# Kernel optimization log

Measured on AMD Instinct MI355X. Metric: run time of the kernel, lower is better.

Reference implementation:

```python
import jax, jax.numpy as jnp
import numpy as np

N_NODES = 50000
N_EDGES = 800000
D_IN = 256
D_OUT = 96


def setup_inputs() -> dict:
    key = jax.random.key(0)
    k1, k2, k3 = jax.random.split(key, 3)
    x = jax.random.normal(k1, (N_NODES, D_IN), dtype=jnp.float32)
    edge_index = jax.random.randint(k2, (2, N_EDGES), 0, N_NODES, dtype=jnp.int64)
    # Glorot-like init for the GCN weight, zeros bias (bias_init=zeros_)
    W = jax.random.normal(k3, (D_IN, D_OUT), dtype=jnp.float32) * (1.0 / np.sqrt(D_IN))
    b = jnp.zeros((D_OUT,), dtype=jnp.float32)
    return {"x": x, "edge_index": edge_index, "W": W, "b": b}


def reference(x, edge_index, W, b):
    # GCNConv with normalize=False, add_self_loops=False:
    #   h = x @ W                      [N, D_OUT]
    #   out[dst] = sum over edges of h[src]
    #   out += bias (added after aggregation)
    src, dst = edge_index[0], edge_index[1]
    h = x @ W                                  # dense projection [N, D_OUT]
    msgs = h[src]                              # gather [E, D_OUT]
    out = jax.ops.segment_sum(msgs, dst, num_segments=x.shape[0])  # scatter-add
    return out + b
```

## Files before the change

### kernel.cpp

```cpp
#include <hip/hip_runtime.h>
#include <hip/hip_bf16.h>

#define N_NODES 50000
#define N_EDGES 800000
#define D_IN 256
#define D_OUT 96

#define NBLK 391
#define NTHR 512
#define CAP  2560
#define EPB  ((N_EDGES + NBLK - 1) / NBLK)
#define EPT  ((EPB + NTHR - 1) / NTHR)
#define WLDS_K 264

typedef short bf16x8 __attribute__((ext_vector_type(8)));
typedef float f32x4 __attribute__((ext_vector_type(4)));

static __device__ inline ushort f2bf(float f) {
    union { __hip_bfloat16 h; ushort s; } u;
    u.h = __float2bfloat16(f);
    return u.s;
}
static __device__ inline float bfhi2f(unsigned int hibits) {
    union { unsigned int u; float f; } v; v.u = hibits; return v.f;
}

__global__ __launch_bounds__(256) void gcn_wt_kernel(
    const float* __restrict__ W, ushort* __restrict__ wT,
    int* __restrict__ bucket_cursor) {
    int c = blockIdx.x;
    int k = threadIdx.x;
    wT[c * D_IN + k] = f2bf(W[k * D_OUT + c]);
    int gid = c * 256 + k;
    if (gid < NBLK) bucket_cursor[gid] = 0;
}

__global__ __launch_bounds__(256) void gcn_gemm_mfma(
    const float* __restrict__ x, const ushort* __restrict__ wT,
    ushort* __restrict__ hB) {
    __shared__ ushort Wlds[96 * WLDS_K];

    const int tid = threadIdx.x;
#pragma unroll
    for (int it = 0; it < 12; ++it) {
        int i   = tid + it * 256;
        int c   = i >> 5;
        int k8  = (i & 31) << 3;
        uint4 v = reinterpret_cast<const uint4*>(wT)[i];
        *reinterpret_cast<uint4*>(&Wlds[c * WLDS_K + k8]) = v;
    }
    __syncthreads();

    const int lane = tid & 63;
    const int wave = tid >> 6;
    const int l15  = lane & 15;
    const int lk   = (lane >> 4) * 8;
    const int arow = blockIdx.x * 64 + wave * 16 + l15;
    const bool aok = arow < N_NODES;
    const float* xrow = &x[(size_t)(aok ? arow : 0) * D_IN];

    f32x4 acc[6];
#pragma unroll
    for (int c = 0; c < 6; ++c) acc[c] = (f32x4){0.f, 0.f, 0.f, 0.f};

#pragma unroll
    for (int kc = 0; kc < D_IN; kc += 32) {
        float4 v0 = make_float4(0.f, 0.f, 0.f, 0.f);
        float4 v1 = make_float4(0.f, 0.f, 0.f, 0.f);
        if (aok) {
            v0 = *reinterpret_cast<const float4*>(&xrow[kc + lk]);
            v1 = *reinterpret_cast<const float4*>(&xrow[kc + lk + 4]);
        }
        bf16x8 a;
        a[0] = (short)f2bf(v0.x); a[1] = (short)f2bf(v0.y);
        a[2] = (short)f2bf(v0.z); a[3] = (short)f2bf(v0.w);
        a[4] = (short)f2bf(v1.x); a[5] = (short)f2bf(v1.y);
        a[6] = (short)f2bf(v1.z); a[7] = (short)f2bf(v1.w);
#pragma unroll
        for (int c = 0; c < 6; ++c) {
            bf16x8 bf = *reinterpret_cast<const bf16x8*>(
                &Wlds[(c * 16 + l15) * WLDS_K + kc + lk]);
            acc[c] = __builtin_amdgcn_mfma_f32_16x16x32_bf16(a, bf, acc[c], 0, 0, 0);
        }
    }

    const int rbase = blockIdx.x * 64 + wave * 16 + (lane >> 4) * 4;
#pragma unroll
    for (int r = 0; r < 4; ++r) {
        int orow = rbase + r;
        if (orow < N_NODES) {
#pragma unroll
            for (int c = 0; c < 6; ++c)
                hB[orow * D_OUT + c * 16 + l15] = f2bf(acc[c][r]);
        }
    }
}

__global__ __launch_bounds__(NTHR) void gcn_partition_kernel(
    const int* __restrict__ ei, int* __restrict__ bucket_cursor,
    unsigned int* __restrict__ recs) {
    __shared__ int lhist[NBLK];
    __shared__ int lbase[NBLK];
    const int t = threadIdx.x;
    for (int i = t; i < NBLK; i += NTHR) lhist[i] = 0;
    __syncthreads();

    const int ebase = blockIdx.x * EPB;
    const int eend  = min(ebase + EPB, N_EDGES);
    int bk[EPT]; int rk[EPT]; unsigned int rec[EPT];
#pragma unroll
    for (int i = 0; i < EPT; ++i) {
        int e = ebase + i * NTHR + t;
        bk[i] = -1;
        if (e < eend) {
            int src = ei[e];
            int dst = ei[N_EDGES + e];
            if ((unsigned)src < (unsigned)N_NODES &&
                (unsigned)dst < (unsigned)N_NODES) {
                bk[i]  = dst >> 7;
                rec[i] = (unsigned)src | ((unsigned)(dst & 127) << 16);
                rk[i]  = atomicAdd(&lhist[bk[i]], 1);
            }
        }
    }
    __syncthreads();
    for (int i = t; i < NBLK; i += NTHR)
        lbase[i] = atomicAdd(&bucket_cursor[i], lhist[i]);
    __syncthreads();
#pragma unroll
    for (int i = 0; i < EPT; ++i) {
        if (bk[i] >= 0) {
            int pos = lbase[bk[i]] + rk[i];
            if (pos < CAP)
                recs[bk[i] * CAP + pos] = rec[i];
        }
    }
}

__global__ __launch_bounds__(NTHR, 4) void gcn_csr_agg_kernel(
    const ushort* __restrict__ hB, const int* __restrict__ bucket_cursor,
    const unsigned int* __restrict__ recs, const float* __restrict__ bias,
    float* __restrict__ out) {
    __shared__ unsigned int srec[CAP];
    __shared__ ushort loc[CAP];
    __shared__ int hist[128];
    __shared__ int scanb[128];
    __shared__ int cur[128];
    const int b = blockIdx.x;
    const int t = threadIdx.x;
    int size = bucket_cursor[b];
    if (size > CAP) size = CAP;

    if (t < 128) hist[t] = 0;
    __syncthreads();
    for (int i = t; i < size; i += NTHR) {
        unsigned int r = recs[b * CAP + i];
        srec[i] = r;
        atomicAdd(&hist[(r >> 16) & 127], 1);
    }
    __syncthreads();
    if (t < 128) scanb[t] = hist[t];
    __syncthreads();
    for (int off = 1; off < 128; off <<= 1) {
        int u = 0;
        if (t < 128 && t >= off) u = scanb[t - off];
        __syncthreads();
        if (t < 128) scanb[t] += u;
        __syncthreads();
    }
    if (t < 128) cur[t] = scanb[t] - hist[t];
    __syncthreads();
    for (int i = t; i < size; i += NTHR) {
        unsigned int r = srec[i];
        int l = (r >> 16) & 127;
        int p = atomicAdd(&cur[l], 1);
        loc[p] = (ushort)(r & 0xffffu);
    }
    __syncthreads();

    const int nl   = t >> 2;
    const int fs   = t & 3;
    const int node = b * 128 + nl;
    if (node >= N_NODES) return;

    int deg   = hist[nl];
    int start = cur[nl] - deg;

    float a[24];
#pragma unroll
    for (int j = 0; j < 24; ++j) a[j] = 0.f;

#define ACC8V(v, B)                                \
    a[B+0] += bfhi2f((v).x << 16);                 \
    a[B+1] += bfhi2f((v).x & 0xffff0000u);         \
    a[B+2] += bfhi2f((v).y << 16);                 \
    a[B+3] += bfhi2f((v).y & 0xffff0000u);         \
    a[B+4] += bfhi2f((v).z << 16);                 \
    a[B+5] += bfhi2f((v).z & 0xffff0000u);         \
    a[B+6] += bfhi2f((v).w << 16);                 \
    a[B+7] += bfhi2f((v).w & 0xffff0000u);

    int i = 0;
    for (; i + 4 <= deg; i += 4) {
        int s0 = loc[start + i + 0];
        int s1 = loc[start + i + 1];
        int s2 = loc[start + i + 2];
        int s3 = loc[start + i + 3];
        const ushort* h0 = &hB[s0 * D_OUT + fs * 24];
        const ushort* h1 = &hB[s1 * D_OUT + fs * 24];
        const ushort* h2 = &hB[s2 * D_OUT + fs * 24];
        const ushort* h3 = &hB[s3 * D_OUT + fs * 24];
        uint4 v00 = *reinterpret_cast<const uint4*>(h0 + 0);
        uint4 v01 = *reinterpret_cast<const uint4*>(h0 + 8);
        uint4 v02 = *reinterpret_cast<const uint4*>(h0 + 16);
        uint4 v10 = *reinterpret_cast<const uint4*>(h1 + 0);
        uint4 v11 = *reinterpret_cast<const uint4*>(h1 + 8);
        uint4 v12 = *reinterpret_cast<const uint4*>(h1 + 16);
        uint4 v20 = *reinterpret_cast<const uint4*>(h2 + 0);
        uint4 v21 = *reinterpret_cast<const uint4*>(h2 + 8);
        uint4 v22 = *reinterpret_cast<const uint4*>(h2 + 16);
        uint4 v30 = *reinterpret_cast<const uint4*>(h3 + 0);
        uint4 v31 = *reinterpret_cast<const uint4*>(h3 + 8);
        uint4 v32 = *reinterpret_cast<const uint4*>(h3 + 16);
        ACC8V(v00, 0); ACC8V(v01, 8); ACC8V(v02, 16);
        ACC8V(v10, 0); ACC8V(v11, 8); ACC8V(v12, 16);
        ACC8V(v20, 0); ACC8V(v21, 8); ACC8V(v22, 16);
        ACC8V(v30, 0); ACC8V(v31, 8); ACC8V(v32, 16);
    }
    for (; i < deg; ++i) {
        int s = loc[start + i];
        const ushort* hp = &hB[s * D_OUT + fs * 24];
        uint4 v0 = *reinterpret_cast<const uint4*>(hp + 0);
        uint4 v1 = *reinterpret_cast<const uint4*>(hp + 8);
        uint4 v2 = *reinterpret_cast<const uint4*>(hp + 16);
        ACC8V(v0, 0); ACC8V(v1, 8); ACC8V(v2, 16);
    }
#undef ACC8V

    const float4* bp = reinterpret_cast<const float4*>(&bias[fs * 24]);
    float* op = &out[node * D_OUT + fs * 24];
#pragma unroll
    for (int j = 0; j < 6; ++j) {
        float4 bv = bp[j];
        float4 o  = make_float4(a[j*4+0] + bv.x, a[j*4+1] + bv.y,
                                a[j*4+2] + bv.z, a[j*4+3] + bv.w);
        *reinterpret_cast<float4*>(op + j * 4) = o;
    }
}

extern "C" void kernel_launch(void* const* d_in, const int* in_sizes, int n_in,
                              void* d_out, int out_size, void* d_ws, size_t ws_size,
                              hipStream_t stream) {
    const float* x  = (const float*)d_in[0];
    const int*   ei = (const int*)d_in[1];
    const float* W  = (const float*)d_in[2];
    const float* b  = (const float*)d_in[3];
    float* out = (float*)d_out;

    char* ws = (char*)d_ws;
    ushort*       hB     = (ushort*)(ws);
    ushort*       wT     = (ushort*)(ws + 9600000);
    int*          cursor = (int*)   (ws + 9649152);
    unsigned int* recs   = (unsigned int*)(ws + 9651200);

    gcn_wt_kernel<<<dim3(96), 256, 0, stream>>>(W, wT, cursor);
    gcn_gemm_mfma<<<dim3((N_NODES + 63) / 64), 256, 0, stream>>>(x, wT, hB);

    gcn_partition_kernel<<<dim3(NBLK), NTHR, 0, stream>>>(ei, cursor, recs);

    gcn_csr_agg_kernel<<<dim3(NBLK), NTHR, 0, stream>>>(hB, cursor, recs, b, out);
}
```

Baseline: 145.8 us.

## Fuse projection GEMM and edge partitioning into a single kernel launch

Merges the MFMA projection kernel and the edge bucketing kernel into one kernel. Each of 391 blocks of 512 threads computes 128 rows of h, then partitions its slice of edges. Shared memory is overlaid with a union. This removes one launch boundary and lets partition work overlap with other blocks' GEMM. The cost is fewer, larger GEMM blocks, which may reduce latency hiding for the x stream.

```diff
diff --git a/kernel.cpp b/kernel.cpp
--- a/kernel.cpp
+++ b/kernel.cpp
@@ -35,104 +35,110 @@
     if (gid < NBLK) bucket_cursor[gid] = 0;
 }
 
-__global__ __launch_bounds__(256) void gcn_gemm_mfma(
+union GemmSh {
+    ushort wlds[96 * WLDS_K];
+    struct { int lhist[NBLK]; int lbase[NBLK]; } p;
+};
+
+__global__ __launch_bounds__(NTHR) void gcn_gemm_part_kernel(
     const float* __restrict__ x, const ushort* __restrict__ wT,
-    ushort* __restrict__ hB) {
-    __shared__ ushort Wlds[96 * WLDS_K];
-
+    const int* __restrict__ ei, int* __restrict__ bucket_cursor,
+    unsigned int* __restrict__ recs, ushort* __restrict__ hB) {
+    __shared__ GemmSh sh;
     const int tid = threadIdx.x;
-#pragma unroll
-    for (int it = 0; it < 12; ++it) {
-        int i   = tid + it * 256;
+    const int blk = blockIdx.x;
+
+#pragma unroll
+    for (int it = 0; it < 6; ++it) {
+        int i   = tid + it * NTHR;
         int c   = i >> 5;
         int k8  = (i & 31) << 3;
         uint4 v = reinterpret_cast<const uint4*>(wT)[i];
-        *reinterpret_cast<uint4*>(&Wlds[c * WLDS_K + k8]) = v;
-    }
-    __syncthreads();
-
-    const int lane = tid & 63;
-    const int wave = tid >> 6;
-    const int l15  = lane & 15;
-    const int lk   = (lane >> 4) * 8;
-    const int arow = blockIdx.x * 64 + wave * 16 + l15;
-    const bool aok = arow < N_NODES;
-    const float* xrow = &x[(size_t)(aok ? arow : 0) * D_IN];
-
-    f32x4 acc[6];
-#pragma unroll
-    for (int c = 0; c < 6; ++c) acc[c] = (f32x4){0.f, 0.f, 0.f, 0.f};
-
-#pragma unroll
-    for (int kc = 0; kc < D_IN; kc += 32) {
-        float4 v0 = make_float4(0.f, 0.f, 0.f, 0.f);
-        float4 v1 = make_float4(0.f, 0.f, 0.f, 0.f);
-        if (aok) {
-            v0 = *reinterpret_cast<const float4*>(&xrow[kc + lk]);
-            v1 = *reinterpret_cast<const float4*>(&xrow[kc + lk + 4]);
-        }
-        bf16x8 a;
-        a[0] = (short)f2bf(v0.x); a[1] = (short)f2bf(v0.y);
-        a[2] = (short)f2bf(v0.z); a[3] = (short)f2bf(v0.w);
-        a[4] = (short)f2bf(v1.x); a[5] = (short)f2bf(v1.y);
-        a[6] = (short)f2bf(v1.z); a[7] = (short)f2bf(v1.w);
-#pragma unroll
-        for (int c = 0; c < 6; ++c) {
-            bf16x8 bf = *reinterpret_cast<const bf16x8*>(
-                &Wlds[(c * 16 + l15) * WLDS_K + kc + lk]);
-            acc[c] = __builtin_amdgcn_mfma_f32_16x16x32_bf16(a, bf, acc[c], 0, 0, 0);
-        }
-    }
-
-    const int rbase = blockIdx.x * 64 + wave * 16 + (lane >> 4) * 4;
-#pragma unroll
-    for (int r = 0; r < 4; ++r) {
-        int orow = rbase + r;
-        if (orow < N_NODES) {
-#pragma unroll
-            for (int c = 0; c < 6; ++c)
-                hB[orow * D_OUT + c * 16 + l15] = f2bf(acc[c][r]);
-        }
-    }
-}
-
-__global__ __launch_bounds__(NTHR) void gcn_partition_kernel(
-    const int* __restrict__ ei, int* __restrict__ bucket_cursor,
-    unsigned int* __restrict__ recs) {
-    __shared__ int lhist[NBLK];
-    __shared__ int lbase[NBLK];
-    const int t = threadIdx.x;
-    for (int i = t; i < NBLK; i += NTHR) lhist[i] = 0;
-    __syncthreads();
-
-    const int ebase = blockIdx.x * EPB;
-    const int eend  = min(ebase + EPB, N_EDGES);
-    int bk[EPT]; int rk[EPT]; unsigned int rec[EPT];
-#pragma unroll
-    for (int i = 0; i < EPT; ++i) {
-        int e = ebase + i * NTHR + t;
-        bk[i] = -1;
-        if (e < eend) {
-            int src = ei[e];
-            int dst = ei[N_EDGES + e];
-            if ((unsigned)src < (unsigned)N_NODES &&
-                (unsigned)dst < (unsigned)N_NODES) {
-                bk[i]  = dst >> 7;
-                rec[i] = (unsigned)src | ((unsigned)(dst & 127) << 16);
-                rk[i]  = atomicAdd(&lhist[bk[i]], 1);
-            }
-        }
-    }
-    __syncthreads();
-    for (int i = t; i < NBLK; i += NTHR)
-        lbase[i] = atomicAdd(&bucket_cursor[i], lhist[i]);
-    __syncthreads();
-#pragma unroll
-    for (int i = 0; i < EPT; ++i) {
-        if (bk[i] >= 0) {
-            int pos = lbase[bk[i]] + rk[i];
-            if (pos < CAP)
-                recs[bk[i] * CAP + pos] = rec[i];
+        *reinterpret_cast<uint4*>(&sh.wlds[c * WLDS_K + k8]) = v;
+    }
+    __syncthreads();
+
+    {
+        const int lane = tid & 63;
+        const int wave = tid >> 6;
+        const int l15  = lane & 15;
+        const int lk   = (lane >> 4) * 8;
+        const int arow = blk * 128 + wave * 16 + l15;
+        const bool aok = arow < N_NODES;
+        const float* xrow = &x[(size_t)(aok ? arow : 0) * D_IN];
+
+        f32x4 acc[6];
+#pragma unroll
+        for (int c = 0; c < 6; ++c) acc[c] = (f32x4){0.f, 0.f, 0.f, 0.f};
+
+#pragma unroll
+        for (int kc = 0; kc < D_IN; kc += 32) {
+            float4 v0 = make_float4(0.f, 0.f, 0.f, 0.f);
+            float4 v1 = make_float4(0.f, 0.f, 0.f, 0.f);
+            if (aok) {
+                v0 = *reinterpret_cast<const float4*>(&xrow[kc + lk]);
+                v1 = *reinterpret_cast<const float4*>(&xrow[kc + lk + 4]);
+            }
+            bf16x8 a;
+            a[0] = (short)f2bf(v0.x); a[1] = (short)f2bf(v0.y);
+            a[2] = (short)f2bf(v0.z); a[3] = (short)f2bf(v0.w);
+            a[4] = (short)f2bf(v1.x); a[5] = (short)f2bf(v1.y);
+            a[6] = (short)f2bf(v1.z); a[7] = (short)f2bf(v1.w);
+#pragma unroll
+            for (int c = 0; c < 6; ++c) {
+                bf16x8 bf = *reinterpret_cast<const bf16x8*>(
+                    &sh.wlds[(c * 16 + l15) * WLDS_K + kc + lk]);
+                acc[c] = __builtin_amdgcn_mfma_f32_16x16x32_bf16(a, bf, acc[c], 0, 0, 0);
+            }
+        }
+
+        const int rbase = blk * 128 + wave * 16 + (lane >> 4) * 4;
+#pragma unroll
+        for (int r = 0; r < 4; ++r) {
+            int orow = rbase + r;
+            if (orow < N_NODES) {
+#pragma unroll
+                for (int c = 0; c < 6; ++c)
+                    hB[orow * D_OUT + c * 16 + l15] = f2bf(acc[c][r]);
+            }
+        }
+    }
+
+    __syncthreads();
+    {
+        const int t = tid;
+        for (int i = t; i < NBLK; i += NTHR) sh.p.lhist[i] = 0;
+        __syncthreads();
+
+        const int ebase = blk * EPB;
+        const int eend  = min(ebase + EPB, N_EDGES);
+        int bk[EPT]; int rk[EPT]; unsigned int rec[EPT];
+#pragma unroll
+        for (int i = 0; i < EPT; ++i) {
+            int e = ebase + i * NTHR + t;
+            bk[i] = -1;
+            if (e < eend) {
+                int src = ei[e];
+                int dst = ei[N_EDGES + e];
+                if ((unsigned)src < (unsigned)N_NODES &&
+                    (unsigned)dst < (unsigned)N_NODES) {
+                    bk[i]  = dst >> 7;
+                    rec[i] = (unsigned)src | ((unsigned)(dst & 127) << 16);
+                    rk[i]  = atomicAdd(&sh.p.lhist[bk[i]], 1);
+                }
+            }
+        }
+        __syncthreads();
+        for (int i = t; i < NBLK; i += NTHR)
+            sh.p.lbase[i] = atomicAdd(&bucket_cursor[i], sh.p.lhist[i]);
+        __syncthreads();
+#pragma unroll
+        for (int i = 0; i < EPT; ++i) {
+            if (bk[i] >= 0) {
+                int pos = sh.p.lbase[bk[i]] + rk[i];
+                if (pos < CAP)
+                    recs[bk[i] * CAP + pos] = rec[i];
+            }
         }
     }
 }
@@ -264,9 +270,8 @@
     unsigned int* recs   = (unsigned int*)(ws + 9651200);
 
     gcn_wt_kernel<<<dim3(96), 256, 0, stream>>>(W, wT, cursor);
-    gcn_gemm_mfma<<<dim3((N_NODES + 63) / 64), 256, 0, stream>>>(x, wT, hB);
-
-    gcn_partition_kernel<<<dim3(NBLK), NTHR, 0, stream>>>(ei, cursor, recs);
+
+    gcn_gemm_part_kernel<<<dim3(NBLK), NTHR, 0, stream>>>(x, wT, ei, cursor, recs, hB);
 
     gcn_csr_agg_kernel<<<dim3(NBLK), NTHR, 0, stream>>>(hB, cursor, recs, b, out);
 }
```

Result: faster. 139.5 us (-4.3%).
